# Optimization experiments

Measured on AMD Instinct MI355X. Metric: run time of the kernel, lower is better.

## Reference

```python
import jax, jax.numpy as jnp
import numpy as np

EPS = 1e-5
B, C, H, W, K = 4, 512, 128, 128, 32


def setup_inputs() -> dict:
    key = jax.random.key(0)
    ks = jax.random.split(key, 12)
    std = 1.0 / ((K * C) ** 0.5)
    return {
        "x": jax.random.normal(ks[0], (B, C, H, W), jnp.float32),
        "conv_w": jax.random.normal(ks[1], (C, C), jnp.float32) * (1.0 / C ** 0.5),
        "bn2_g": jnp.ones((C,), jnp.float32),
        "bn2_b": jnp.zeros((C,), jnp.float32),
        "bn2_m": jax.random.normal(ks[2], (C,), jnp.float32) * 0.1,
        "bn2_v": jax.random.uniform(ks[3], (C,), jnp.float32) + 0.5,
        "codewords": jax.random.uniform(ks[4], (K, C), jnp.float32, -std, std),
        "scale": jax.random.uniform(ks[5], (K,), jnp.float32, -1.0, 0.0),
        "bn1_g": jnp.ones((K,), jnp.float32),
        "bn1_b": jnp.zeros((K,), jnp.float32),
        "bn1_m": jax.random.normal(ks[6], (K,), jnp.float32) * 0.1,
        "bn1_v": jax.random.uniform(ks[7], (K,), jnp.float32) + 0.5,
        "fc_w": jax.random.normal(ks[8], (C, C), jnp.float32) * (1.0 / C ** 0.5),
        "fc_b": jnp.zeros((C,), jnp.float32),
    }


def _encoding(z, codewords, scale):
    # z: [B,N,C], codewords: [K,C], scale: [K]
    # scaled L2: scale_k * ||z_n - c_k||^2, expanded to avoid the [B,N,K,C] tensor
    x2 = jnp.sum(z * z, axis=-1, keepdims=True)          # [B,N,1]
    c2 = jnp.sum(codewords * codewords, axis=-1)         # [K]
    xc = jnp.einsum('bnc,kc->bnk', z, codewords)         # [B,N,K]
    scaled_l2 = scale * (x2 - 2.0 * xc + c2)             # [B,N,K]
    assign = jax.nn.softmax(scaled_l2, axis=-1)          # softmax over codes
    # aggregate: sum_n assign[b,n,k] * (z[b,n,:] - c[k,:])
    agg = jnp.einsum('bnk,bnc->bkc', assign, z) \
        - jnp.sum(assign, axis=1)[..., None] * codewords  # [B,K,C]
    return agg


def reference(x, conv_w, bn2_g, bn2_b, bn2_m, bn2_v, codewords, scale,
              bn1_g, bn1_b, bn1_m, bn1_v, fc_w, fc_b):
    b, c, h, w = x.shape
    # encoding_project: 1x1 conv (no bias) + BN2d (eval) + ReLU
    p = jnp.einsum('bchw,oc->bohw', x, conv_w)
    p = (p - bn2_m[None, :, None, None]) * jax.lax.rsqrt(bn2_v + EPS)[None, :, None, None] \
        * bn2_g[None, :, None, None] + bn2_b[None, :, None, None]
    p = jax.nn.relu(p)
    z = p.reshape(b, c, h * w).transpose(0, 2, 1)        # [B,N,C]
    e = _encoding(z, codewords, scale)                   # [B,K,C]
    # BN1d over num_codes (eval), broadcast over channel dim, then ReLU
    e = (e - bn1_m[None, :, None]) * jax.lax.rsqrt(bn1_v + EPS)[None, :, None] \
        * bn1_g[None, :, None] + bn1_b[None, :, None]
    e = jax.nn.relu(e)
    feat = e.mean(axis=1)                                # [B,C]
    gamma = jax.nn.sigmoid(feat @ fc_w.T + fc_b)         # [B,C]
    out = jax.nn.relu(x + x * gamma[:, :, None, None])   # channel gate + residual
    return feat, out
```

## Files before the change

kernel.cpp:

```cpp
#include <hip/hip_runtime.h>
#include <cstdint>

#define EPS 1e-5f
constexpr int B = 4, C = 512, HW = 16384, K = 32;

typedef __bf16 bf16x8 __attribute__((ext_vector_type(8)));
typedef float  floatx4 __attribute__((ext_vector_type(4)));
typedef unsigned int u32;

__device__ __forceinline__ void load_lds16(const void* g, void* l) {
    __builtin_amdgcn_global_load_lds((const __attribute__((address_space(1))) u32*)g,
                                     (__attribute__((address_space(3))) u32*)l,
                                     16, 0, 0);
}

constexpr size_t Z_OFF     = 0;
constexpr size_t WBB_OFF   = 67108864;
constexpr size_t CWB_OFF   = 67633152;
constexpr size_t X2_OFF    = 67665920;
constexpr size_t C2_OFF    = 67928064;
constexpr size_t ASUM_OFF  = 67928192;
constexpr size_t PART_OFF  = 67928704;
constexpr size_t AGG_OFF   = 101483136;
constexpr size_t GAMMA_OFF = 101745280;

__global__ __launch_bounds__(256) void prep_kernel(
    const float* __restrict__ conv_w, const float* __restrict__ cw,
    __bf16* __restrict__ wbb, __bf16* __restrict__ cwb,
    float* __restrict__ c2, float* __restrict__ asum) {
    const int tid = threadIdx.x, bx = blockIdx.x;
    if (bx < 128) {
        const int idx  = bx * 256 + tid;
        const int lane = idx & 63;
        const int ks   = (idx >> 6) & 1;
        const int ii   = (idx >> 7) & 7;
        const int t    = idx >> 10;
        const float* s = conv_w + (size_t)(t * 16 + (lane & 15)) * C
                         + ii * 64 + ks * 32 + (lane >> 4) * 8;
        bf16x8 o;
        #pragma unroll
        for (int j = 0; j < 8; j++) o[j] = (__bf16)s[j];
        *(bf16x8*)&wbb[(size_t)idx * 8] = o;
    } else if (bx < 132) {
        const int idx = ((bx - 128) * 256 + tid) * 16;
        const float* s = cw + idx;
        __bf16* d = cwb + idx;
        bf16x8 o0, o1;
        #pragma unroll
        for (int j = 0; j < 8; j++) o0[j] = (__bf16)s[j];
        #pragma unroll
        for (int j = 0; j < 8; j++) o1[j] = (__bf16)s[8 + j];
        *(bf16x8*)&d[0] = o0;
        *(bf16x8*)&d[8] = o1;
    } else {
        if (tid < 32) {
            const float* r = cw + tid * 512;
            float s = 0.f;
            for (int c = 0; c < 512; c++) s += r[c] * r[c];
            c2[tid] = s;
        }
        if (tid < 128) asum[tid] = 0.f;
    }
}

__global__ __launch_bounds__(256) void conv_fused_kernel(
    const float* __restrict__ x, const __bf16* __restrict__ wbb,
    const float* __restrict__ g2, const float* __restrict__ b2,
    const float* __restrict__ m2, const float* __restrict__ v2,
    __bf16* __restrict__ z, float* __restrict__ x2g) {
    __shared__ float  XR[2][64 * 64];
    __shared__ __bf16 XA[64 * 72];
    __shared__ float  x2L[64];
    const int tid = threadIdx.x, lane = tid & 63, w = tid >> 6;
    const int l15 = lane & 15, q = lane >> 4;
    const int n0 = blockIdx.x * 64, b = blockIdx.y;
    if (tid < 64) x2L[tid] = 0.f;

    auto stage = [&](int chunk, int buf) {
        #pragma unroll
        for (int p = 0; p < 4; p++) {
            int seg = w * 4 + p;
            int cr = chunk * 64 + seg * 4 + (lane >> 4);
            const float* gp = x + ((size_t)(b * C + cr)) * HW + n0 + (lane & 15) * 4;
            load_lds16(gp, (char*)XR[buf] + seg * 1024);
        }
    };

    floatx4 acc[4][8];
    const floatx4 zv4 = {0.f, 0.f, 0.f, 0.f};
    #pragma unroll
    for (int mt = 0; mt < 4; mt++)
        #pragma unroll
        for (int ot = 0; ot < 8; ot++) acc[mt][ot] = zv4;

    stage(0, 0);
    for (int i = 0; i < 8; i++) {
        const int cur = i & 1;
        __syncthreads();
        if (i < 7) stage(i + 1, cur ^ 1);
        #pragma unroll
        for (int f = 0; f < 2; f++) {
            int id = f * 256 + tid;
            int n = id & 63, cs = id >> 6;
            bf16x8 o;
            #pragma unroll
            for (int j = 0; j < 8; j++) o[j] = (__bf16)XR[cur][(cs * 8 + j) * 64 + n];
            *(bf16x8*)&XA[n * 72 + cs * 8] = o;
        }
        asm volatile("s_waitcnt lgkmcnt(0)" ::: "memory");
        __builtin_amdgcn_sched_barrier(0);
        __builtin_amdgcn_s_barrier();
        __builtin_amdgcn_sched_barrier(0);
        #pragma unroll
        for (int ks = 0; ks < 2; ks++) {
            bf16x8 af[4], bfv[8];
            #pragma unroll
            for (int ot = 0; ot < 8; ot++)
                bfv[ot] = *(const bf16x8*)&wbb[
                    ((size_t)(((w * 8 + ot) * 8 + i) * 2 + ks) * 64 + lane) * 8];
            #pragma unroll
            for (int mt = 0; mt < 4; mt++)
                af[mt] = *(const bf16x8*)&XA[(mt * 16 + l15) * 72 + ks * 32 + q * 8];
            #pragma unroll
            for (int mt = 0; mt < 4; mt++)
                #pragma unroll
                for (int ot = 0; ot < 8; ot++)
                    acc[mt][ot] = __builtin_amdgcn_mfma_f32_16x16x32_bf16(
                        af[mt], bfv[ot], acc[mt][ot], 0, 0, 0);
        }
    }
    float s8[8], bi8[8];
    #pragma unroll
    for (int ot = 0; ot < 8; ot++) {
        int o = w * 128 + ot * 16 + l15;
        float s = g2[o] * rsqrtf(v2[o] + EPS);
        s8[ot] = s; bi8[ot] = b2[o] - m2[o] * s;
    }
    float xx[16];
    #pragma unroll
    for (int t = 0; t < 16; t++) xx[t] = 0.f;
    #pragma unroll
    for (int mt = 0; mt < 4; mt++)
        #pragma unroll
        for (int reg = 0; reg < 4; reg++) {
            int n = n0 + mt * 16 + q * 4 + reg;
            #pragma unroll
            for (int ot = 0; ot < 8; ot++) {
                float v = fmaxf(acc[mt][ot][reg] * s8[ot] + bi8[ot], 0.f);
                z[((size_t)(b * HW + n)) * C + w * 128 + ot * 16 + l15] = (__bf16)v;
                xx[mt * 4 + reg] += v * v;
            }
        }
    #pragma unroll
    for (int t = 0; t < 16; t++) {
        float v = xx[t];
        v += __shfl_xor(v, 1); v += __shfl_xor(v, 2);
        v += __shfl_xor(v, 4); v += __shfl_xor(v, 8);
        xx[t] = v;
    }
    if (l15 == 0) {
        #pragma unroll
        for (int mt = 0; mt < 4; mt++)
            #pragma unroll
            for (int reg = 0; reg < 4; reg++)
                atomicAdd(&x2L[mt * 16 + q * 4 + reg], xx[mt * 4 + reg]);
    }
    __syncthreads();
    if (tid < 64) x2g[(size_t)b * HW + n0 + tid] = x2L[tid];
}

__global__ __launch_bounds__(256) void assign_agg_kernel(
    const __bf16* __restrict__ zb, const __bf16* __restrict__ cwb,
    const float* __restrict__ scale, const float* __restrict__ c2,
    const float* __restrict__ x2g, float* __restrict__ part,
    float* __restrict__ asum) {
    __shared__ __bf16 ZT[32][528];
    __shared__ float  LG[32][33];
    __shared__ __bf16 AT[32][40];
    __shared__ float  asum_l[32];
    const int tid = threadIdx.x, lane = tid & 63, w = tid >> 6;
    const int l15 = lane & 15, q = lane >> 4;
    const int b = blockIdx.y, bx = blockIdx.x;
    if (tid < 32) asum_l[tid] = 0.f;
    float sck[8], c2k[8];
    #pragma unroll
    for (int j = 0; j < 8; j++) { sck[j] = scale[q * 8 + j]; c2k[j] = c2[q * 8 + j]; }
    const int mt_ = w >> 1, nt_ = w & 1;

    floatx4 agga[2][8];
    const floatx4 zv4 = {0.f, 0.f, 0.f, 0.f};
    #pragma unroll
    for (int mt = 0; mt < 2; mt++)
        #pragma unroll
        for (int ct = 0; ct < 8; ct++) agga[mt][ct] = zv4;

    for (int s = 0; s < 4; s++) {
        const int nb = bx * 128 + s * 32;
        bf16x8 st[8];
        #pragma unroll
        for (int p = 0; p < 8; p++) {
            int e = (p * 256 + tid) * 8;
            int n = e >> 9, c = e & 511;
            st[p] = *(const bf16x8*)&zb[((size_t)(b * HW + nb + n)) * C + c];
        }
        __syncthreads();
        #pragma unroll
        for (int p = 0; p < 8; p++) {
            int e = (p * 256 + tid) * 8;
            int n = e >> 9, c = e & 511;
            *(bf16x8*)&ZT[n][c] = st[p];
        }
        __syncthreads();
        floatx4 la = zv4;
        #pragma unroll
        for (int kc = 0; kc < 16; kc++) {
            bf16x8 a  = *(const bf16x8*)&cwb[(size_t)(mt_ * 16 + l15) * C + kc * 32 + q * 8];
            bf16x8 bb = *(const bf16x8*)&ZT[nt_ * 16 + l15][kc * 32 + q * 8];
            la = __builtin_amdgcn_mfma_f32_16x16x32_bf16(a, bb, la, 0, 0, 0);
        }
        #pragma unroll
        for (int r = 0; r < 4; r++)
            LG[mt_ * 16 + q * 4 + r][nt_ * 16 + l15] = la[r];
        __syncthreads();
        if (w < 2) {
            int nl = w * 16 + l15;
            float x2v = x2g[(size_t)b * HW + nb + nl];
            float lg[8];
            float mx = -1e30f;
            #pragma unroll
            for (int j = 0; j < 8; j++) {
                float t = sck[j] * (x2v - 2.f * LG[q * 8 + j][nl] + c2k[j]);
                lg[j] = t; mx = fmaxf(mx, t);
            }
            mx = fmaxf(mx, __shfl_xor(mx, 16));
            mx = fmaxf(mx, __shfl_xor(mx, 32));
            float se = 0.f;
            #pragma unroll
            for (int j = 0; j < 8; j++) { lg[j] = __expf(lg[j] - mx); se += lg[j]; }
            se += __shfl_xor(se, 16);
            se += __shfl_xor(se, 32);
            float inv = 1.f / se;
            #pragma unroll
            for (int j = 0; j < 8; j++) {
                float a = lg[j] * inv;
                AT[q * 8 + j][nl] = (__bf16)a;
                lg[j] = a;
            }
            #pragma unroll
            for (int j = 0; j < 8; j++) {
                float v = lg[j];
                v += __shfl_xor(v, 1); v += __shfl_xor(v, 2);
                v += __shfl_xor(v, 4); v += __shfl_xor(v, 8);
                if (l15 == 0) atomicAdd(&asum_l[q * 8 + j], v);
            }
        }
        __syncthreads();
        bf16x8 afr0 = *(const bf16x8*)&AT[l15][q * 8];
        bf16x8 afr1 = *(const bf16x8*)&AT[16 + l15][q * 8];
        #pragma unroll
        for (int ct = 0; ct < 8; ct++) {
            int c = w * 128 + ct * 16 + l15;
            bf16x8 bb;
            #pragma unroll
            for (int j = 0; j < 8; j++) bb[j] = ZT[q * 8 + j][c];
            agga[0][ct] = __builtin_amdgcn_mfma_f32_16x16x32_bf16(afr0, bb, agga[0][ct], 0, 0, 0);
            agga[1][ct] = __builtin_amdgcn_mfma_f32_16x16x32_bf16(afr1, bb, agga[1][ct], 0, 0, 0);
        }
    }
    float* pp = part + ((size_t)(b * 128 + bx) * K) * C;
    #pragma unroll
    for (int mt = 0; mt < 2; mt++)
        #pragma unroll
        for (int ct = 0; ct < 8; ct++)
            #pragma unroll
            for (int r = 0; r < 4; r++)
                pp[(size_t)(mt * 16 + q * 4 + r) * C + w * 128 + ct * 16 + l15] =
                    agga[mt][ct][r];
    __syncthreads();
    if (tid < 32) atomicAdd(&asum[b * K + tid], asum_l[tid]);
}

__global__ __launch_bounds__(512) void agg_reduce_kernel(
    const float* __restrict__ part, float* __restrict__ agg) {
    const int k = blockIdx.x, b = blockIdx.y, c = threadIdx.x;
    float s = 0.f;
    for (int p = 0; p < 128; p++)
        s += part[((size_t)((b * 128 + p) * K + k)) * C + c];
    agg[((size_t)(b * K + k)) * C + c] = s;
}

__global__ __launch_bounds__(512) void feat_kernel(
    const float* __restrict__ cw,
    const float* __restrict__ g1, const float* __restrict__ b1,
    const float* __restrict__ m1, const float* __restrict__ v1,
    const float* __restrict__ fcw, const float* __restrict__ fcb,
    const float* __restrict__ agg, const float* __restrict__ asum,
    float* __restrict__ gamma, float* __restrict__ out_feat) {
    __shared__ float featL[C];
    const int tid = threadIdx.x;
    const int b = blockIdx.x;
    float f = 0.f;
    for (int kk = 0; kk < K; kk++) {
        float s = g1[kk] * rsqrtf(v1[kk] + EPS);
        float bias = b1[kk] - m1[kk] * s;
        float e = agg[((size_t)b * K + kk) * C + tid] - asum[b * K + kk] * cw[kk * C + tid];
        f += fmaxf(e * s + bias, 0.f);
    }
    f *= (1.f / 32.f);
    out_feat[b * C + tid] = f;
    featL[tid] = f;
    __syncthreads();
    const int w = tid >> 6, l = tid & 63;
    for (int cc = w * 64; cc < w * 64 + 64; cc++) {
        const float* row = &fcw[(size_t)cc * C + l * 8];
        float4 fa = *(const float4*)&featL[l * 8];
        float4 fb = *(const float4*)&featL[l * 8 + 4];
        float4 wa = *(const float4*)row;
        float4 wb = *(const float4*)(row + 4);
        float s = fa.x * wa.x + fa.y * wa.y + fa.z * wa.z + fa.w * wa.w
                + fb.x * wb.x + fb.y * wb.y + fb.z * wb.z + fb.w * wb.w;
        #pragma unroll
        for (int d = 32; d >= 1; d >>= 1) s += __shfl_xor(s, d);
        if (l == 0) gamma[b * C + cc] = 1.f / (1.f + __expf(-(s + fcb[cc])));
    }
}

__global__ __launch_bounds__(256) void gate_kernel(const float* __restrict__ x,
                                                   const float* __restrict__ gamma,
                                                   float* __restrict__ out) {
    size_t idx = (size_t)blockIdx.x * 256 + threadIdx.x;
    int bc = (int)(idx >> 12);
    float gm = 1.f + gamma[bc];
    float4 xv = ((const float4*)x)[idx];
    float4 r;
    r.x = fmaxf(xv.x * gm, 0.f);
    r.y = fmaxf(xv.y * gm, 0.f);
    r.z = fmaxf(xv.z * gm, 0.f);
    r.w = fmaxf(xv.w * gm, 0.f);
    ((float4*)out)[idx] = r;
}

extern "C" void kernel_launch(void* const* d_in, const int* in_sizes, int n_in,
                              void* d_out, int out_size, void* d_ws, size_t ws_size,
                              hipStream_t stream) {
    const float* x      = (const float*)d_in[0];
    const float* conv_w = (const float*)d_in[1];
    const float* bn2_g  = (const float*)d_in[2];
    const float* bn2_b  = (const float*)d_in[3];
    const float* bn2_m  = (const float*)d_in[4];
    const float* bn2_v  = (const float*)d_in[5];
    const float* cw     = (const float*)d_in[6];
    const float* scale  = (const float*)d_in[7];
    const float* bn1_g  = (const float*)d_in[8];
    const float* bn1_b  = (const float*)d_in[9];
    const float* bn1_m  = (const float*)d_in[10];
    const float* bn1_v  = (const float*)d_in[11];
    const float* fcw    = (const float*)d_in[12];
    const float* fcb    = (const float*)d_in[13];
    char* wsb = (char*)d_ws;
    __bf16* zbuf  = (__bf16*)(wsb + Z_OFF);
    __bf16* wbb   = (__bf16*)(wsb + WBB_OFF);
    __bf16* cwb   = (__bf16*)(wsb + CWB_OFF);
    float*  x2    = (float*)(wsb + X2_OFF);
    float*  c2    = (float*)(wsb + C2_OFF);
    float*  asum  = (float*)(wsb + ASUM_OFF);
    float*  part  = (float*)(wsb + PART_OFF);
    float*  agg   = (float*)(wsb + AGG_OFF);
    float*  gamma = (float*)(wsb + GAMMA_OFF);
    float* out = (float*)d_out;

    prep_kernel<<<133, 256, 0, stream>>>(conv_w, cw, wbb, cwb, c2, asum);
    conv_fused_kernel<<<dim3(256, 4), 256, 0, stream>>>(
        x, wbb, bn2_g, bn2_b, bn2_m, bn2_v, zbuf, x2);
    assign_agg_kernel<<<dim3(128, 4), 256, 0, stream>>>(
        zbuf, cwb, scale, c2, x2, part, asum);
    agg_reduce_kernel<<<dim3(32, 4), 512, 0, stream>>>(part, agg);
    feat_kernel<<<4, 512, 0, stream>>>(cw, bn1_g, bn1_b, bn1_m, bn1_v,
                                       fcw, fcb, agg, asum, gamma, out);
    gate_kernel<<<32768, 256, 0, stream>>>(x, gamma, out + B * C);
}
```

Before: 448.9 us.

## Pre-transpose x to swizzled bf16 layout before the 1x1 conv GEMM

Adds a transpose kernel that converts x from fp32 [B,C,N] into a bf16, XOR-swizzled [B,chunk,N,64] layout in workspace. The conv kernel then streams ready-to-use bf16 tiles straight into LDS with direct global-to-LDS loads, dropping the in-kernel fp32-to-bf16 conversion and transpose. It also halves its LDS footprint and raises the occupancy target. The cost is an extra kernel launch plus writing and re-reading a 64 MB intermediate. The original conv kernel is kept as a fallback when the workspace is too small.

```diff
diff --git a/kernel.cpp b/kernel.cpp
--- a/kernel.cpp
+++ b/kernel.cpp
@@ -23,6 +23,9 @@
 constexpr size_t PART_OFF  = 67928704;
 constexpr size_t AGG_OFF   = 101483136;
 constexpr size_t GAMMA_OFF = 101745280;
+constexpr size_t XT_OFF    = 101753472;
+constexpr size_t XT_BYTES  = (size_t)B * 8 * 16384 * 64 * 2;
+constexpr size_t WS_NEEDED = XT_OFF + XT_BYTES;
 
 __global__ __launch_bounds__(256) void prep_kernel(
     const float* __restrict__ conv_w, const float* __restrict__ cw,
@@ -63,7 +66,138 @@
     }
 }
 
-__global__ __launch_bounds__(256) void conv_fused_kernel(
+__global__ __launch_bounds__(512) void xpose_kernel(
+    const float* __restrict__ x, __bf16* __restrict__ xt) {
+    __shared__ float XR[64 * 256];
+    const int tid = threadIdx.x, lane = tid & 63, wv = tid >> 6;
+    const int nt = blockIdx.x, chunk = blockIdx.y, b = blockIdx.z;
+    #pragma unroll
+    for (int p = 0; p < 8; p++) {
+        int r = wv * 8 + p;
+        int s = (r & 7) ^ ((r >> 3) & 7);
+        const float* gp = x + ((size_t)(b * C + chunk * 64 + r)) * HW
+                          + nt * 256 + ((lane ^ s) * 4);
+        load_lds16(gp, (char*)XR + r * 1024);
+    }
+    __syncthreads();
+    const int c8 = tid & 7;
+    #pragma unroll
+    for (int k = 0; k < 4; k++) {
+        int nloc = (tid >> 3) + k * 64;
+        bf16x8 o;
+        #pragma unroll
+        for (int j = 0; j < 8; j++) {
+            int cl = c8 * 8 + j;
+            int g  = (nloc >> 2) ^ (j ^ c8);
+            o[j] = (__bf16)XR[cl * 256 + g * 4 + (nloc & 3)];
+        }
+        size_t rowbase = ((size_t)(b * 8 + chunk) * 16384 + nt * 256 + nloc) * 64;
+        *(bf16x8*)&xt[rowbase + ((c8 ^ (nloc & 7)) * 8)] = o;
+    }
+}
+
+__global__ __launch_bounds__(256, 3) void conv_fused_v3_kernel(
+    const __bf16* __restrict__ xt, const __bf16* __restrict__ wbb,
+    const float* __restrict__ g2, const float* __restrict__ b2,
+    const float* __restrict__ m2, const float* __restrict__ v2,
+    __bf16* __restrict__ z, float* __restrict__ x2g) {
+    __shared__ __bf16 XA[2][64 * 64];
+    __shared__ float  x2L[64];
+    const int tid = threadIdx.x, lane = tid & 63, w = tid >> 6;
+    const int l15 = lane & 15, q = lane >> 4;
+    const int n0 = blockIdx.x * 64, b = blockIdx.y;
+    if (tid < 64) x2L[tid] = 0.f;
+
+    auto stage = [&](int chunk, int buf) {
+        #pragma unroll
+        for (int p = 0; p < 2; p++) {
+            int seg = w * 2 + p;
+            const __bf16* gp = xt + ((size_t)(b * 8 + chunk) * 16384 + n0 + seg * 8) * 64
+                               + lane * 8;
+            load_lds16(gp, (char*)XA[buf] + seg * 1024);
+        }
+    };
+
+    floatx4 acc[4][8];
+    const floatx4 zv4 = {0.f, 0.f, 0.f, 0.f};
+    #pragma unroll
+    for (int mt = 0; mt < 4; mt++)
+        #pragma unroll
+        for (int ot = 0; ot < 8; ot++) acc[mt][ot] = zv4;
+
+    stage(0, 0);
+    for (int i = 0; i < 8; i++) {
+        const int buf = i & 1;
+        __syncthreads();
+        if (i < 7) stage(i + 1, buf ^ 1);
+        #pragma unroll
+        for (int ks = 0; ks < 2; ks++) {
+            bf16x8 af[4];
+            #pragma unroll
+            for (int mt = 0; mt < 4; mt++) {
+                int row = mt * 16 + l15;
+                af[mt] = *(const bf16x8*)((const char*)XA[buf]
+                          + row * 128 + (((ks * 4 + q) ^ (row & 7)) * 16));
+            }
+            #pragma unroll
+            for (int og = 0; og < 2; og++) {
+                bf16x8 bfv[4];
+                #pragma unroll
+                for (int o4 = 0; o4 < 4; o4++) {
+                    int ot = og * 4 + o4;
+                    bfv[o4] = *(const bf16x8*)&wbb[
+                        ((size_t)(((w * 8 + ot) * 8 + i) * 2 + ks) * 64 + lane) * 8];
+                }
+                #pragma unroll
+                for (int mt = 0; mt < 4; mt++)
+                    #pragma unroll
+                    for (int o4 = 0; o4 < 4; o4++)
+                        acc[mt][og * 4 + o4] = __builtin_amdgcn_mfma_f32_16x16x32_bf16(
+                            af[mt], bfv[o4], acc[mt][og * 4 + o4], 0, 0, 0);
+            }
+        }
+    }
+    float s8[8], bi8[8];
+    #pragma unroll
+    for (int ot = 0; ot < 8; ot++) {
+        int o = w * 128 + ot * 16 + l15;
+        float s = g2[o] * rsqrtf(v2[o] + EPS);
+        s8[ot] = s; bi8[ot] = b2[o] - m2[o] * s;
+    }
+    float xx[16];
+    #pragma unroll
+    for (int t = 0; t < 16; t++) xx[t] = 0.f;
+    #pragma unroll
+    for (int mt = 0; mt < 4; mt++)
+        #pragma unroll
+        for (int reg = 0; reg < 4; reg++) {
+            int n = n0 + mt * 16 + q * 4 + reg;
+            #pragma unroll
+            for (int ot = 0; ot < 8; ot++) {
+                float v = fmaxf(acc[mt][ot][reg] * s8[ot] + bi8[ot], 0.f);
+                z[((size_t)(b * HW + n)) * C + w * 128 + ot * 16 + l15] = (__bf16)v;
+                xx[mt * 4 + reg] += v * v;
+            }
+        }
+    #pragma unroll
+    for (int t = 0; t < 16; t++) {
+        float v = xx[t];
+        v += __shfl_xor(v, 1); v += __shfl_xor(v, 2);
+        v += __shfl_xor(v, 4); v += __shfl_xor(v, 8);
+        xx[t] = v;
+    }
+    if (l15 == 0) {
+        #pragma unroll
+        for (int mt = 0; mt < 4; mt++)
+            #pragma unroll
+            for (int reg = 0; reg < 4; reg++)
+                atomicAdd(&x2L[mt * 16 + q * 4 + reg], xx[mt * 4 + reg]);
+    }
+    __syncthreads();
+    if (tid < 64) x2g[(size_t)b * HW + n0 + tid] = x2L[tid];
+}
+
+__global__ __launch_bounds__(256) void conv_fused_fb_kernel(
     const float* __restrict__ x, const __bf16* __restrict__ wbb,
     const float* __restrict__ g2, const float* __restrict__ b2,
     const float* __restrict__ m2, const float* __restrict__ v2,
@@ -367,11 +501,18 @@
     float*  part  = (float*)(wsb + PART_OFF);
     float*  agg   = (float*)(wsb + AGG_OFF);
     float*  gamma = (float*)(wsb + GAMMA_OFF);
+    __bf16* xt    = (__bf16*)(wsb + XT_OFF);
     float* out = (float*)d_out;
 
     prep_kernel<<<133, 256, 0, stream>>>(conv_w, cw, wbb, cwb, c2, asum);
-    conv_fused_kernel<<<dim3(256, 4), 256, 0, stream>>>(
-        x, wbb, bn2_g, bn2_b, bn2_m, bn2_v, zbuf, x2);
+    if (ws_size >= WS_NEEDED) {
+        xpose_kernel<<<dim3(64, 8, 4), 512, 0, stream>>>(x, xt);
+        conv_fused_v3_kernel<<<dim3(256, 4), 256, 0, stream>>>(
+            xt, wbb, bn2_g, bn2_b, bn2_m, bn2_v, zbuf, x2);
+    } else {
+        conv_fused_fb_kernel<<<dim3(256, 4), 256, 0, stream>>>(
+            x, wbb, bn2_g, bn2_b, bn2_m, bn2_v, zbuf, x2);
+    }
     assign_agg_kernel<<<dim3(128, 4), 256, 0, stream>>>(
         zbuf, cwb, scale, c2, x2, part, asum);
     agg_reduce_kernel<<<dim3(32, 4), 512, 0, stream>>>(part, agg);
```

New measurement: 656.6 us. 1.46x slower.

## Prefetch next Z tile into registers and relax barriers in assign_agg kernel

Applied to the files above, without the earlier changes.

Software-pipelines the assign/aggregate loop: the next 32-row Z tile is loaded from global memory into registers while the current tile is computed. Most __syncthreads are replaced with explicit lgkmcnt waits plus s_barrier, so the barrier no longer waits on outstanding global loads. The per-row x2 values are hoisted into registers before the loop, and the ZT row pitch is padded from 528 to 536 to change the LDS bank mapping. This adds register pressure and relies on hand-placed wait and barrier ordering being correct.

```diff
diff --git a/kernel.cpp b/kernel.cpp
--- a/kernel.cpp
+++ b/kernel.cpp
@@ -174,7 +174,7 @@
     const float* __restrict__ scale, const float* __restrict__ c2,
     const float* __restrict__ x2g, float* __restrict__ part,
     float* __restrict__ asum) {
-    __shared__ __bf16 ZT[32][528];
+    __shared__ __bf16 ZT[32][536];
     __shared__ float  LG[32][33];
     __shared__ __bf16 AT[32][40];
     __shared__ float  asum_l[32];
@@ -187,6 +187,13 @@
     for (int j = 0; j < 8; j++) { sck[j] = scale[q * 8 + j]; c2k[j] = c2[q * 8 + j]; }
     const int mt_ = w >> 1, nt_ = w & 1;
 
+    float x2r[4];
+    if (w < 2) {
+        #pragma unroll
+        for (int s = 0; s < 4; s++)
+            x2r[s] = x2g[(size_t)b * HW + bx * 128 + s * 32 + w * 16 + l15];
+    }
+
     floatx4 agga[2][8];
     const floatx4 zv4 = {0.f, 0.f, 0.f, 0.f};
     #pragma unroll
@@ -194,23 +201,33 @@
         #pragma unroll
         for (int ct = 0; ct < 8; ct++) agga[mt][ct] = zv4;
 
+    bf16x8 st[8];
+    #pragma unroll
+    for (int p = 0; p < 8; p++) {
+        int e = (p * 256 + tid) * 8;
+        st[p] = *(const bf16x8*)&zb[((size_t)(b * HW + bx * 128 + (e >> 9))) * C + (e & 511)];
+    }
+
     for (int s = 0; s < 4; s++) {
         const int nb = bx * 128 + s * 32;
-        bf16x8 st[8];
+        __syncthreads();
         #pragma unroll
         for (int p = 0; p < 8; p++) {
             int e = (p * 256 + tid) * 8;
-            int n = e >> 9, c = e & 511;
-            st[p] = *(const bf16x8*)&zb[((size_t)(b * HW + nb + n)) * C + c];
-        }
-        __syncthreads();
-        #pragma unroll
-        for (int p = 0; p < 8; p++) {
-            int e = (p * 256 + tid) * 8;
-            int n = e >> 9, c = e & 511;
-            *(bf16x8*)&ZT[n][c] = st[p];
-        }
-        __syncthreads();
+            *(bf16x8*)&ZT[e >> 9][e & 511] = st[p];
+        }
+        if (s < 3) {
+            #pragma unroll
+            for (int p = 0; p < 8; p++) {
+                int e = (p * 256 + tid) * 8;
+                st[p] = *(const bf16x8*)&zb[
+                    ((size_t)(b * HW + nb + 32 + (e >> 9))) * C + (e & 511)];
+            }
+        }
+        asm volatile("s_waitcnt lgkmcnt(0)" ::: "memory");
+        __builtin_amdgcn_sched_barrier(0);
+        __builtin_amdgcn_s_barrier();
+        __builtin_amdgcn_sched_barrier(0);
         floatx4 la = zv4;
         #pragma unroll
         for (int kc = 0; kc < 16; kc++) {
@@ -221,15 +238,17 @@
         #pragma unroll
         for (int r = 0; r < 4; r++)
             LG[mt_ * 16 + q * 4 + r][nt_ * 16 + l15] = la[r];
-        __syncthreads();
+        asm volatile("s_waitcnt lgkmcnt(0)" ::: "memory");
+        __builtin_amdgcn_sched_barrier(0);
+        __builtin_amdgcn_s_barrier();
+        __builtin_amdgcn_sched_barrier(0);
         if (w < 2) {
             int nl = w * 16 + l15;
-            float x2v = x2g[(size_t)b * HW + nb + nl];
             float lg[8];
             float mx = -1e30f;
             #pragma unroll
             for (int j = 0; j < 8; j++) {
-                float t = sck[j] * (x2v - 2.f * LG[q * 8 + j][nl] + c2k[j]);
+                float t = sck[j] * (x2r[s] - 2.f * LG[q * 8 + j][nl] + c2k[j]);
                 lg[j] = t; mx = fmaxf(mx, t);
             }
             mx = fmaxf(mx, __shfl_xor(mx, 16));
@@ -254,7 +273,10 @@
                 if (l15 == 0) atomicAdd(&asum_l[q * 8 + j], v);
             }
         }
-        __syncthreads();
+        asm volatile("s_waitcnt lgkmcnt(0)" ::: "memory");
+        __builtin_amdgcn_sched_barrier(0);
+        __builtin_amdgcn_s_barrier();
+        __builtin_amdgcn_sched_barrier(0);
         bf16x8 afr0 = *(const bf16x8*)&AT[l15][q * 8];
         bf16x8 afr1 = *(const bf16x8*)&AT[16 + l15][q * 8];
         #pragma unroll
```

Result: slower. 459.2 us (+2.3%).
